# Kernel tuning notes

Hardware: AMD Instinct MI355X
Metric: run time of the kernel (lower is better)

Reference implementation:

```python
import jax, jax.numpy as jnp
import numpy as np

N_NODES = 100_000
N_EDGES = 3_200_000
F_IN = 64
HID = 16
N_CLASSES = 4


def setup_inputs() -> dict:
    key = jax.random.key(0)
    ks = jax.random.split(key, 9)
    x = jax.random.normal(ks[0], (N_NODES, F_IN), dtype=jnp.float32)
    edge_index = jax.random.randint(ks[1], (2, N_EDGES), 0, N_NODES, dtype=jnp.int64)
    edge_weight = jax.random.uniform(ks[2], (N_EDGES,), dtype=jnp.float32)
    # Glorot-style init for the three GCN layer weights, zero bias (PyG default)
    W1 = jax.random.normal(ks[3], (F_IN, HID), dtype=jnp.float32) * (1.0 / np.sqrt(F_IN))
    b1 = jnp.zeros((HID,), jnp.float32)
    W3 = jax.random.normal(ks[4], (HID, HID), dtype=jnp.float32) * (1.0 / np.sqrt(HID))
    b3 = jnp.zeros((HID,), jnp.float32)
    W2 = jax.random.normal(ks[5], (HID, N_CLASSES), dtype=jnp.float32) * (1.0 / np.sqrt(HID))
    b2 = jnp.zeros((N_CLASSES,), jnp.float32)
    return {"x": x, "edge_index": edge_index, "edge_weight": edge_weight,
            "W1": W1, "b1": b1, "W3": W3, "b3": b3, "W2": W2, "b2": b2}


def reference(x, edge_index, edge_weight, W1, b1, W3, b3, W2, b2):
    n = x.shape[0]
    # GCNConv default: add self-loops with weight 1, symmetric deg^-1/2 norm
    loop = jnp.arange(n, dtype=edge_index.dtype)
    row = jnp.concatenate([edge_index[0], loop])  # source nodes
    col = jnp.concatenate([edge_index[1], loop])  # target nodes
    ew = jnp.concatenate([edge_weight, jnp.ones((n,), edge_weight.dtype)])
    deg = jax.ops.segment_sum(ew, col, num_segments=n)
    dinv = jnp.where(deg > 0, jax.lax.rsqrt(deg), 0.0)
    norm = dinv[row] * ew * dinv[col]  # [E+N]

    def gcn_conv(h, W, b):
        h = h @ W                                  # [N, out] small matmul first
        msg = norm[:, None] * h[row]               # gather + scale, [E+N, out]
        return jax.ops.segment_sum(msg, col, num_segments=n) + b

    h = jax.nn.relu(gcn_conv(x, W1, b1))
    # dropout is identity in eval mode (training=False)
    h = jax.nn.relu(gcn_conv(h, W3, b3))
    h = gcn_conv(h, W2, b2)
    return jax.nn.log_softmax(h, axis=1)
```

## Files before the change

kernel.cpp:

```cpp
#include <hip/hip_runtime.h>
#include <math.h>

#define NN 100000
#define NE 3200000
#define F_IN 64
#define HID 16
#define NC 4

#define SZB 256
#define NB 391
#define CAP 10240
#define CH 8192
#define NCH 391
#define NW 16

typedef _Float16 half_t;
typedef _Float16 h4f __attribute__((ext_vector_type(4)));

__device__ __forceinline__ float upw(int pk) {
    unsigned short us = (unsigned short)(pk & 0x7fff);
    half_t h;
    __builtin_memcpy(&h, &us, 2);
    return (float)h;
}

__global__ __launch_bounds__(1024) void k_bin(const int* __restrict__ row,
                                              const int* __restrict__ col,
                                              const float* __restrict__ ew,
                                              int* __restrict__ cursor,
                                              uint2* __restrict__ bin) {
    __shared__ int h[NB];
    __shared__ int lstart[NB + 1];
    __shared__ int gbase[NB];
    __shared__ int ps[512];
    __shared__ uint2 stage[CH];
    int tid = threadIdx.x;
    for (int i = tid; i < NB; i += 1024) h[i] = 0;
    __syncthreads();
    int e0 = blockIdx.x * CH;
    int e1 = min(e0 + CH, NE);
    int eCnt = e1 - e0;
    for (int i = e0 + tid * 4; i < e1; i += 1024 * 4) {
        int4 c4 = *(const int4*)(col + i);
        atomicAdd(&h[c4.x >> 8], 1);
        atomicAdd(&h[c4.y >> 8], 1);
        atomicAdd(&h[c4.z >> 8], 1);
        atomicAdd(&h[c4.w >> 8], 1);
    }
    __syncthreads();
    int c0 = (tid < NB) ? h[tid] : 0;
    if (tid < 512) ps[tid] = c0;
    for (int off = 1; off < 512; off <<= 1) {
        __syncthreads();
        int v = (tid < 512 && tid >= off) ? ps[tid - off] : 0;
        __syncthreads();
        if (tid < 512) ps[tid] += v;
    }
    __syncthreads();
    if (tid < NB) {
        int ex = ps[tid] - c0;
        lstart[tid] = ex;
        h[tid] = ex;
        if (c0) gbase[tid] = tid * CAP + atomicAdd(&cursor[tid], c0);
    }
    if (tid == 0) lstart[NB] = eCnt;
    __syncthreads();
    for (int i = e0 + tid * 4; i < e1; i += 1024 * 4) {
        int4 c4 = *(const int4*)(col + i);
        int4 r4 = *(const int4*)(row + i);
        float4 w4 = *(const float4*)(ew + i);
        int p;
        p = atomicAdd(&h[c4.x >> 8], 1);
        stage[p] = make_uint2(((unsigned)r4.x << 8) | (c4.x & 255), __float_as_uint(w4.x));
        p = atomicAdd(&h[c4.y >> 8], 1);
        stage[p] = make_uint2(((unsigned)r4.y << 8) | (c4.y & 255), __float_as_uint(w4.y));
        p = atomicAdd(&h[c4.z >> 8], 1);
        stage[p] = make_uint2(((unsigned)r4.z << 8) | (c4.z & 255), __float_as_uint(w4.z));
        p = atomicAdd(&h[c4.w >> 8], 1);
        stage[p] = make_uint2(((unsigned)r4.w << 8) | (c4.w & 255), __float_as_uint(w4.w));
    }
    __syncthreads();
    for (int i = tid; i < eCnt; i += 1024) {
        int lo = 0, hi = NB;
        while (hi - lo > 1) {
            int mid = (lo + hi) >> 1;
            if (lstart[mid] <= i) lo = mid; else hi = mid;
        }
        int d = gbase[lo] + (i - lstart[lo]);
        if (d < (lo + 1) * CAP)
            bin[d] = stage[i];
    }
}

__global__ __launch_bounds__(1024) void k_sort(const uint2* __restrict__ bin,
                                               const int* __restrict__ cursor,
                                               const float* __restrict__ x,
                                               const float* __restrict__ W1,
                                               unsigned* __restrict__ epk,
                                               int2* __restrict__ nodeptr2,
                                               float* __restrict__ dinv,
                                               half_t* __restrict__ tt1) {
    __shared__ int hw[NW][SZB];
    __shared__ int cnt[SZB];
    __shared__ int ps[SZB];
    __shared__ unsigned stage[CAP];
    __shared__ float Ws[F_IN * HID];
    int b = blockIdx.x, tid = threadIdx.x;
    int w = tid >> 6;
    for (int i = tid; i < NW * SZB; i += 1024) ((int*)hw)[i] = 0;
    for (int i = tid; i < F_IN * HID; i += 1024) Ws[i] = W1[i];
    __syncthreads();
    int s = b * CAP;
    int m = min(cursor[b], CAP);
    int e = s + m;
    for (int i = s + tid; i < e; i += 1024)
        atomicAdd(&hw[w][bin[i].x & 255], 1);
    __syncthreads();
    if (tid < SZB) {
        int c = 0;
#pragma unroll
        for (int ww = 0; ww < NW; ww++) c += hw[ww][tid];
        cnt[tid] = c;
    }
    __syncthreads();
    int pc = (tid < SZB) ? ((cnt[tid] + 3) & ~3) : 0;
    if (tid < SZB) ps[tid] = pc;
    for (int off = 1; off < SZB; off <<= 1) {
        __syncthreads();
        int v = (tid < SZB && tid >= off) ? ps[tid - off] : 0;
        __syncthreads();
        if (tid < SZB) ps[tid] += v;
    }
    __syncthreads();
    if (tid < SZB) {
        int run = ps[tid] - pc;
#pragma unroll
        for (int ww = 0; ww < NW; ww++) {
            int t = hw[ww][tid];
            hw[ww][tid] = run;
            run += t;
        }
    }
    __syncthreads();
    int mpad = min(ps[SZB - 1], CAP);
    for (int i = tid; i < mpad; i += 1024) stage[i] = 0u;
    __syncthreads();
    for (int i = s + tid; i < e; i += 1024) {
        uint2 u = bin[i];
        int cl = u.x & 255;
        int pos = atomicAdd(&hw[w][cl], 1);
        half_t hwt = (half_t)__uint_as_float(u.y);
        unsigned short hb;
        __builtin_memcpy(&hb, &hwt, 2);
        if (pos < CAP)
            stage[pos] = ((u.x >> 8) << 15) | (unsigned)(hb & 0x7fff);
    }
    __syncthreads();
    for (int i = tid; i < mpad; i += 1024) epk[s + i] = stage[i];
    int nl = tid >> 2, l = tid & 3;
    int n = b * SZB + nl;
    int pcn = (cnt[nl] + 3) & ~3;
    int ex = ps[nl] - pcn;
    float sw = 0.0f;
    for (int i = ex + l; i < ex + pcn; i += 4) sw += upw((int)stage[i]);
    sw += __shfl_xor(sw, 1, 4);
    sw += __shfl_xor(sw, 2, 4);
    float di = rsqrtf(1.0f + sw);
    if (n < NN && l == 0) {
        nodeptr2[n] = make_int2(s + ex, s + ex + pcn);
        dinv[n] = di;
    }
    if (n < NN) {
        float part[HID];
#pragma unroll
        for (int j = 0; j < HID; j++) part[j] = 0.0f;
        const float4* xp = (const float4*)(x + (size_t)n * F_IN) + l * 4;
#pragma unroll
        for (int k4 = 0; k4 < 4; k4++) {
            float4 v = xp[k4];
            int k = l * 16 + k4 * 4;
#pragma unroll
            for (int j = 0; j < HID; j++) {
                part[j] += v.x * Ws[(k + 0) * HID + j];
                part[j] += v.y * Ws[(k + 1) * HID + j];
                part[j] += v.z * Ws[(k + 2) * HID + j];
                part[j] += v.w * Ws[(k + 3) * HID + j];
            }
        }
#pragma unroll
        for (int j = 0; j < HID; j++) {
            part[j] += __shfl_xor(part[j], 1, 4);
            part[j] += __shfl_xor(part[j], 2, 4);
        }
        h4f o;
        o.x = (half_t)(di * part[4 * l + 0]);
        o.y = (half_t)(di * part[4 * l + 1]);
        o.z = (half_t)(di * part[4 * l + 2]);
        o.w = (half_t)(di * part[4 * l + 3]);
        ((h4f*)tt1)[n * 4 + l] = o;
    }
}

template <int DN>
__global__ __launch_bounds__(256) void k_aggf(const unsigned* __restrict__ epk,
                                              const int2* __restrict__ nptr,
                                              const half_t* __restrict__ tt_in,
                                              const float* __restrict__ bias,
                                              const float* __restrict__ dinv,
                                              const float* __restrict__ Wn,
                                              half_t* __restrict__ tt_out) {
    __shared__ float Ws[HID * DN];
    if (threadIdx.x < HID * DN) Ws[threadIdx.x] = Wn[threadIdx.x];
    __syncthreads();
    int tid = blockIdx.x * 256 + threadIdx.x;
    int n = tid >> 2;
    int l = tid & 3;
    if (n >= NN) return;
    int2 p = nptr[n];
    const h4f* ttp = (const h4f*)tt_in;
    h4f sv = ttp[n * 4 + l];
    float ax = 0.f, ay = 0.f, az = 0.f, aw = 0.f;
    for (int base = p.x; base < p.y; base += 4) {
        int4 q = *(const int4*)(epk + base);
        int r0 = ((unsigned)q.x) >> 15;
        int r1 = ((unsigned)q.y) >> 15;
        int r2 = ((unsigned)q.z) >> 15;
        int r3 = ((unsigned)q.w) >> 15;
        float w0 = upw(q.x), w1 = upw(q.y), w2 = upw(q.z), w3 = upw(q.w);
        h4f v0 = ttp[r0 * 4 + l];
        h4f v1 = ttp[r1 * 4 + l];
        h4f v2 = ttp[r2 * 4 + l];
        h4f v3 = ttp[r3 * 4 + l];
        ax += w0 * (float)v0.x; ay += w0 * (float)v0.y; az += w0 * (float)v0.z; aw += w0 * (float)v0.w;
        ax += w1 * (float)v1.x; ay += w1 * (float)v1.y; az += w1 * (float)v1.z; aw += w1 * (float)v1.w;
        ax += w2 * (float)v2.x; ay += w2 * (float)v2.y; az += w2 * (float)v2.z; aw += w2 * (float)v2.w;
        ax += w3 * (float)v3.x; ay += w3 * (float)v3.y; az += w3 * (float)v3.z; aw += w3 * (float)v3.w;
    }
    float di = dinv[n];
    const float4* b4p = (const float4*)bias;
    float4 b4 = b4p[l];
    float hreg[4];
    hreg[0] = fmaxf(b4.x + di * (ax + (float)sv.x), 0.f);
    hreg[1] = fmaxf(b4.y + di * (ay + (float)sv.y), 0.f);
    hreg[2] = fmaxf(b4.z + di * (az + (float)sv.z), 0.f);
    hreg[3] = fmaxf(b4.w + di * (aw + (float)sv.w), 0.f);
    if (DN == 16) {
        float ox = 0.f, oy = 0.f, oz = 0.f, ow = 0.f;
#pragma unroll
        for (int k = 0; k < HID; k++) {
            float hk = __shfl(hreg[k & 3], k >> 2, 4);
            const float4 wk = *(const float4*)&Ws[k * 16 + 4 * l];
            ox += hk * wk.x; oy += hk * wk.y; oz += hk * wk.z; ow += hk * wk.w;
        }
        h4f ov;
        ov.x = (half_t)(di * ox); ov.y = (half_t)(di * oy);
        ov.z = (half_t)(di * oz); ov.w = (half_t)(di * ow);
        ((h4f*)tt_out)[n * 4 + l] = ov;
    } else {
        float o = 0.f;
#pragma unroll
        for (int k = 0; k < HID; k++) {
            float hk = __shfl(hreg[k & 3], k >> 2, 4);
            o += hk * Ws[k * DN + l];
        }
        tt_out[(size_t)n * DN + l] = (half_t)(di * o);
    }
}

__global__ __launch_bounds__(256) void k_agg4sm(const unsigned* __restrict__ epk,
                                                const int2* __restrict__ nptr,
                                                const half_t* __restrict__ tt,
                                                const float* __restrict__ bias,
                                                const float* __restrict__ dinv,
                                                float* __restrict__ out) {
    int tid = blockIdx.x * 256 + threadIdx.x;
    int n = tid >> 2;
    int l = tid & 3;
    if (n >= NN) return;
    int2 p = nptr[n];
    float self = (float)tt[n * 4 + l];
    float acc = 0.f;
    for (int base = p.x; base < p.y; base += 4) {
        int4 q = *(const int4*)(epk + base);
        int r0 = ((unsigned)q.x) >> 15;
        int r1 = ((unsigned)q.y) >> 15;
        int r2 = ((unsigned)q.z) >> 15;
        int r3 = ((unsigned)q.w) >> 15;
        acc += upw(q.x) * (float)tt[r0 * 4 + l];
        acc += upw(q.y) * (float)tt[r1 * 4 + l];
        acc += upw(q.z) * (float)tt[r2 * 4 + l];
        acc += upw(q.w) * (float)tt[r3 * 4 + l];
    }
    float di = dinv[n];
    float logit = bias[l] + di * (acc + self);
    float m = logit;
    m = fmaxf(m, __shfl_xor(m, 1, 4));
    m = fmaxf(m, __shfl_xor(m, 2, 4));
    float ex = expf(logit - m);
    float s = ex;
    s += __shfl_xor(s, 1, 4);
    s += __shfl_xor(s, 2, 4);
    out[n * 4 + l] = logit - m - logf(s);
}

extern "C" void kernel_launch(void* const* d_in, const int* in_sizes, int n_in,
                              void* d_out, int out_size, void* d_ws, size_t ws_size,
                              hipStream_t stream) {
    const float* x  = (const float*)d_in[0];
    const int*   ei = (const int*)d_in[1];
    const float* ew = (const float*)d_in[2];
    const float* W1 = (const float*)d_in[3];
    const float* b1 = (const float*)d_in[4];
    const float* W3 = (const float*)d_in[5];
    const float* b3 = (const float*)d_in[6];
    const float* W2 = (const float*)d_in[7];
    const float* b2 = (const float*)d_in[8];
    float* out = (float*)d_out;

    const int* row = ei;
    const int* col = ei + NE;

    const size_t NEP = (size_t)NB * CAP;
    char* ws = (char*)d_ws;
    size_t off = 0;
    float*    dinv     = (float*)(ws + off);    off += 400000;
    int2*     nodeptr2 = (int2*)(ws + off);     off += 800000;
    int*      cursor   = (int*)(ws + off);      off += 2048;
    unsigned* epk      = (unsigned*)(ws + off); off += NEP * 4;
    uint2*    bin      = (uint2*)(ws + off);    off += NEP * 8;
    half_t*   tt1      = (half_t*)(ws + off);   off += (size_t)NN * HID * 2;
    half_t*   tt2      = (half_t*)(ws + off);   off += (size_t)NN * HID * 2;
    half_t*   tt3      = (half_t*)(ws + off);   off += (size_t)NN * NC * 2;

    hipMemsetAsync(cursor, 0, NB * sizeof(int), stream);

    k_bin<<<NCH, 1024, 0, stream>>>(row, col, ew, cursor, bin);
    k_sort<<<NB, 1024, 0, stream>>>(bin, cursor, x, W1, epk, nodeptr2, dinv, tt1);

    int gA = (NN * 4 + 255) / 256;

    k_aggf<HID><<<gA, 256, 0, stream>>>(epk, nodeptr2, tt1, b1, dinv, W3, tt2);
    k_aggf<NC><<<gA, 256, 0, stream>>>(epk, nodeptr2, tt2, b3, dinv, W2, tt3);
    k_agg4sm<<<gA, 256, 0, stream>>>(epk, nodeptr2, tt3, b2, dinv, out);
}
```

Baseline: 233.3 us.

## Split binned edges into key/fp16 arrays and use 2 threads per node in aggregation

```diff
diff --git a/kernel.cpp b/kernel.cpp
--- a/kernel.cpp
+++ b/kernel.cpp
@@ -15,7 +15,9 @@
 #define NW 16
 
 typedef _Float16 half_t;
+typedef _Float16 h2f __attribute__((ext_vector_type(2)));
 typedef _Float16 h4f __attribute__((ext_vector_type(4)));
+typedef _Float16 h8f __attribute__((ext_vector_type(8)));
 
 __device__ __forceinline__ float upw(int pk) {
     unsigned short us = (unsigned short)(pk & 0x7fff);
@@ -28,12 +30,14 @@
                                               const int* __restrict__ col,
                                               const float* __restrict__ ew,
                                               int* __restrict__ cursor,
-                                              uint2* __restrict__ bin) {
+                                              unsigned* __restrict__ bkey,
+                                              half_t* __restrict__ bw) {
     __shared__ int h[NB];
     __shared__ int lstart[NB + 1];
     __shared__ int gbase[NB];
     __shared__ int ps[512];
-    __shared__ uint2 stage[CH];
+    __shared__ unsigned skey_st[CH];
+    __shared__ half_t sw_st[CH];
     int tid = threadIdx.x;
     for (int i = tid; i < NB; i += 1024) h[i] = 0;
     __syncthreads();
@@ -71,13 +75,13 @@
         float4 w4 = *(const float4*)(ew + i);
         int p;
         p = atomicAdd(&h[c4.x >> 8], 1);
-        stage[p] = make_uint2(((unsigned)r4.x << 8) | (c4.x & 255), __float_as_uint(w4.x));
+        skey_st[p] = ((unsigned)r4.x << 8) | (c4.x & 255); sw_st[p] = (half_t)w4.x;
         p = atomicAdd(&h[c4.y >> 8], 1);
-        stage[p] = make_uint2(((unsigned)r4.y << 8) | (c4.y & 255), __float_as_uint(w4.y));
+        skey_st[p] = ((unsigned)r4.y << 8) | (c4.y & 255); sw_st[p] = (half_t)w4.y;
         p = atomicAdd(&h[c4.z >> 8], 1);
-        stage[p] = make_uint2(((unsigned)r4.z << 8) | (c4.z & 255), __float_as_uint(w4.z));
+        skey_st[p] = ((unsigned)r4.z << 8) | (c4.z & 255); sw_st[p] = (half_t)w4.z;
         p = atomicAdd(&h[c4.w >> 8], 1);
-        stage[p] = make_uint2(((unsigned)r4.w << 8) | (c4.w & 255), __float_as_uint(w4.w));
+        skey_st[p] = ((unsigned)r4.w << 8) | (c4.w & 255); sw_st[p] = (half_t)w4.w;
     }
     __syncthreads();
     for (int i = tid; i < eCnt; i += 1024) {
@@ -87,12 +91,15 @@
             if (lstart[mid] <= i) lo = mid; else hi = mid;
         }
         int d = gbase[lo] + (i - lstart[lo]);
-        if (d < (lo + 1) * CAP)
-            bin[d] = stage[i];
-    }
-}
-
-__global__ __launch_bounds__(1024) void k_sort(const uint2* __restrict__ bin,
+        if (d < (lo + 1) * CAP) {
+            bkey[d] = skey_st[i];
+            bw[d] = sw_st[i];
+        }
+    }
+}
+
+__global__ __launch_bounds__(1024) void k_sort(const unsigned* __restrict__ bkey,
+                                               const half_t* __restrict__ bw,
                                                const int* __restrict__ cursor,
                                                const float* __restrict__ x,
                                                const float* __restrict__ W1,
@@ -114,7 +121,7 @@
     int m = min(cursor[b], CAP);
     int e = s + m;
     for (int i = s + tid; i < e; i += 1024)
-        atomicAdd(&hw[w][bin[i].x & 255], 1);
+        atomicAdd(&hw[w][bkey[i] & 255], 1);
     __syncthreads();
     if (tid < SZB) {
         int c = 0;
@@ -146,14 +153,14 @@
     for (int i = tid; i < mpad; i += 1024) stage[i] = 0u;
     __syncthreads();
     for (int i = s + tid; i < e; i += 1024) {
-        uint2 u = bin[i];
-        int cl = u.x & 255;
+        unsigned k = bkey[i];
+        int cl = k & 255;
         int pos = atomicAdd(&hw[w][cl], 1);
-        half_t hwt = (half_t)__uint_as_float(u.y);
+        half_t hwt = bw[i];
         unsigned short hb;
         __builtin_memcpy(&hb, &hwt, 2);
         if (pos < CAP)
-            stage[pos] = ((u.x >> 8) << 15) | (unsigned)(hb & 0x7fff);
+            stage[pos] = ((k >> 8) << 15) | (unsigned)(hb & 0x7fff);
     }
     __syncthreads();
     for (int i = tid; i < mpad; i += 1024) epk[s + i] = stage[i];
@@ -213,13 +220,15 @@
     if (threadIdx.x < HID * DN) Ws[threadIdx.x] = Wn[threadIdx.x];
     __syncthreads();
     int tid = blockIdx.x * 256 + threadIdx.x;
-    int n = tid >> 2;
-    int l = tid & 3;
+    int n = tid >> 1;
+    int l = tid & 1;
     if (n >= NN) return;
     int2 p = nptr[n];
-    const h4f* ttp = (const h4f*)tt_in;
-    h4f sv = ttp[n * 4 + l];
-    float ax = 0.f, ay = 0.f, az = 0.f, aw = 0.f;
+    const h8f* ttp = (const h8f*)tt_in;
+    h8f sv = ttp[n * 2 + l];
+    float a[8];
+#pragma unroll
+    for (int j = 0; j < 8; j++) a[j] = 0.0f;
     for (int base = p.x; base < p.y; base += 4) {
         int4 q = *(const int4*)(epk + base);
         int r0 = ((unsigned)q.x) >> 15;
@@ -227,43 +236,49 @@
         int r2 = ((unsigned)q.z) >> 15;
         int r3 = ((unsigned)q.w) >> 15;
         float w0 = upw(q.x), w1 = upw(q.y), w2 = upw(q.z), w3 = upw(q.w);
-        h4f v0 = ttp[r0 * 4 + l];
-        h4f v1 = ttp[r1 * 4 + l];
-        h4f v2 = ttp[r2 * 4 + l];
-        h4f v3 = ttp[r3 * 4 + l];
-        ax += w0 * (float)v0.x; ay += w0 * (float)v0.y; az += w0 * (float)v0.z; aw += w0 * (float)v0.w;
-        ax += w1 * (float)v1.x; ay += w1 * (float)v1.y; az += w1 * (float)v1.z; aw += w1 * (float)v1.w;
-        ax += w2 * (float)v2.x; ay += w2 * (float)v2.y; az += w2 * (float)v2.z; aw += w2 * (float)v2.w;
-        ax += w3 * (float)v3.x; ay += w3 * (float)v3.y; az += w3 * (float)v3.z; aw += w3 * (float)v3.w;
+        h8f v0 = ttp[r0 * 2 + l];
+        h8f v1 = ttp[r1 * 2 + l];
+        h8f v2 = ttp[r2 * 2 + l];
+        h8f v3 = ttp[r3 * 2 + l];
+#pragma unroll
+        for (int j = 0; j < 8; j++) {
+            a[j] += w0 * (float)v0[j];
+            a[j] += w1 * (float)v1[j];
+            a[j] += w2 * (float)v2[j];
+            a[j] += w3 * (float)v3[j];
+        }
     }
     float di = dinv[n];
-    const float4* b4p = (const float4*)bias;
-    float4 b4 = b4p[l];
-    float hreg[4];
-    hreg[0] = fmaxf(b4.x + di * (ax + (float)sv.x), 0.f);
-    hreg[1] = fmaxf(b4.y + di * (ay + (float)sv.y), 0.f);
-    hreg[2] = fmaxf(b4.z + di * (az + (float)sv.z), 0.f);
-    hreg[3] = fmaxf(b4.w + di * (aw + (float)sv.w), 0.f);
+    float hreg[8];
+#pragma unroll
+    for (int j = 0; j < 8; j++)
+        hreg[j] = fmaxf(bias[8 * l + j] + di * (a[j] + (float)sv[j]), 0.f);
     if (DN == 16) {
-        float ox = 0.f, oy = 0.f, oz = 0.f, ow = 0.f;
+        float o[8];
+#pragma unroll
+        for (int j = 0; j < 8; j++) o[j] = 0.0f;
 #pragma unroll
         for (int k = 0; k < HID; k++) {
-            float hk = __shfl(hreg[k & 3], k >> 2, 4);
-            const float4 wk = *(const float4*)&Ws[k * 16 + 4 * l];
-            ox += hk * wk.x; oy += hk * wk.y; oz += hk * wk.z; ow += hk * wk.w;
-        }
-        h4f ov;
-        ov.x = (half_t)(di * ox); ov.y = (half_t)(di * oy);
-        ov.z = (half_t)(di * oz); ov.w = (half_t)(di * ow);
-        ((h4f*)tt_out)[n * 4 + l] = ov;
+            float hk = __shfl(hreg[k & 7], k >> 3, 2);
+#pragma unroll
+            for (int j = 0; j < 8; j++) o[j] += hk * Ws[k * 16 + 8 * l + j];
+        }
+        h8f ov;
+#pragma unroll
+        for (int j = 0; j < 8; j++) ov[j] = (half_t)(di * o[j]);
+        ((h8f*)tt_out)[n * 2 + l] = ov;
     } else {
-        float o = 0.f;
+        float o0 = 0.f, o1 = 0.f;
 #pragma unroll
         for (int k = 0; k < HID; k++) {
-            float hk = __shfl(hreg[k & 3], k >> 2, 4);
-            o += hk * Ws[k * DN + l];
-        }
-        tt_out[(size_t)n * DN + l] = (half_t)(di * o);
+            float hk = __shfl(hreg[k & 7], k >> 3, 2);
+            o0 += hk * Ws[k * DN + 2 * l + 0];
+            o1 += hk * Ws[k * DN + 2 * l + 1];
+        }
+        h2f ov;
+        ov.x = (half_t)(di * o0);
+        ov.y = (half_t)(di * o1);
+        ((h2f*)tt_out)[n * 2 + l] = ov;
     }
 }
 
@@ -274,33 +289,39 @@
                                                 const float* __restrict__ dinv,
                                                 float* __restrict__ out) {
     int tid = blockIdx.x * 256 + threadIdx.x;
-    int n = tid >> 2;
-    int l = tid & 3;
+    int n = tid >> 1;
+    int l = tid & 1;
     if (n >= NN) return;
     int2 p = nptr[n];
-    float self = (float)tt[n * 4 + l];
-    float acc = 0.f;
+    const h2f* ttp = (const h2f*)tt;
+    h2f sv = ttp[n * 2 + l];
+    float a0 = 0.f, a1 = 0.f;
     for (int base = p.x; base < p.y; base += 4) {
         int4 q = *(const int4*)(epk + base);
         int r0 = ((unsigned)q.x) >> 15;
         int r1 = ((unsigned)q.y) >> 15;
         int r2 = ((unsigned)q.z) >> 15;
         int r3 = ((unsigned)q.w) >> 15;
-        acc += upw(q.x) * (float)tt[r0 * 4 + l];
-        acc += upw(q.y) * (float)tt[r1 * 4 + l];
-        acc += upw(q.z) * (float)tt[r2 * 4 + l];
-        acc += upw(q.w) * (float)tt[r3 * 4 + l];
+        float w0 = upw(q.x), w1 = upw(q.y), w2 = upw(q.z), w3 = upw(q.w);
+        h2f v0 = ttp[r0 * 2 + l];
+        h2f v1 = ttp[r1 * 2 + l];
+        h2f v2 = ttp[r2 * 2 + l];
+        h2f v3 = ttp[r3 * 2 + l];
+        a0 += w0 * (float)v0.x; a1 += w0 * (float)v0.y;
+        a0 += w1 * (float)v1.x; a1 += w1 * (float)v1.y;
+        a0 += w2 * (float)v2.x; a1 += w2 * (float)v2.y;
+        a0 += w3 * (float)v3.x; a1 += w3 * (float)v3.y;
     }
     float di = dinv[n];
-    float logit = bias[l] + di * (acc + self);
-    float m = logit;
-    m = fmaxf(m, __shfl_xor(m, 1, 4));
-    m = fmaxf(m, __shfl_xor(m, 2, 4));
-    float ex = expf(logit - m);
-    float s = ex;
-    s += __shfl_xor(s, 1, 4);
-    s += __shfl_xor(s, 2, 4);
-    out[n * 4 + l] = logit - m - logf(s);
+    float lg0 = bias[2 * l + 0] + di * (a0 + (float)sv.x);
+    float lg1 = bias[2 * l + 1] + di * (a1 + (float)sv.y);
+    float m = fmaxf(lg0, lg1);
+    m = fmaxf(m, __shfl_xor(m, 1, 2));
+    float s = expf(lg0 - m) + expf(lg1 - m);
+    s += __shfl_xor(s, 1, 2);
+    float ls = m + logf(s);
+    float2 o = make_float2(lg0 - ls, lg1 - ls);
+    ((float2*)out)[n * 2 + l] = o;
 }
 
 extern "C" void kernel_launch(void* const* d_in, const int* in_sizes, int n_in,
@@ -327,19 +348,20 @@
     int2*     nodeptr2 = (int2*)(ws + off);     off += 800000;
     int*      cursor   = (int*)(ws + off);      off += 2048;
     unsigned* epk      = (unsigned*)(ws + off); off += NEP * 4;
-    uint2*    bin      = (uint2*)(ws + off);    off += NEP * 8;
+    unsigned* bkey     = (unsigned*)(ws + off); off += NEP * 4;
+    half_t*   bw       = (half_t*)(ws + off);   off += NEP * 2;
     half_t*   tt1      = (half_t*)(ws + off);   off += (size_t)NN * HID * 2;
     half_t*   tt2      = (half_t*)(ws + off);   off += (size_t)NN * HID * 2;
     half_t*   tt3      = (half_t*)(ws + off);   off += (size_t)NN * NC * 2;
 
     hipMemsetAsync(cursor, 0, NB * sizeof(int), stream);
 
-    k_bin<<<NCH, 1024, 0, stream>>>(row, col, ew, cursor, bin);
-    k_sort<<<NB, 1024, 0, stream>>>(bin, cursor, x, W1, epk, nodeptr2, dinv, tt1);
-
-    int gA = (NN * 4 + 255) / 256;
-
-    k_aggf<HID><<<gA, 256, 0, stream>>>(epk, nodeptr2, tt1, b1, dinv, W3, tt2);
-    k_aggf<NC><<<gA, 256, 0, stream>>>(epk, nodeptr2, tt2, b3, dinv, W2, tt3);
-    k_agg4sm<<<gA, 256, 0, stream>>>(epk, nodeptr2, tt3, b2, dinv, out);
-}
+    k_bin<<<NCH, 1024, 0, stream>>>(row, col, ew, cursor, bkey, bw);
+    k_sort<<<NB, 1024, 0, stream>>>(bkey, bw, cursor, x, W1, epk, nodeptr2, dinv, tt1);
+
+    int gA2 = (NN * 2 + 255) / 256;
+
+    k_aggf<HID><<<gA2, 256, 0, stream>>>(epk, nodeptr2, tt1, b1, dinv, W3, tt2);
+    k_aggf<NC><<<gA2, 256, 0, stream>>>(epk, nodeptr2, tt2, b3, dinv, W2, tt3);
+    k_agg4sm<<<gA2, 256, 0, stream>>>(epk, nodeptr2, tt3, b2, dinv, out);
+}
```

Measured after the change: 244.7 us. 1.05x slower.
